# Kernel tuning notes

Measured on AMD Instinct MI355X. Metric: run time of the kernel, lower is better.

## Reference

```python
import jax, jax.numpy as jnp
import numpy as np

N, E = 50000, 800000
F_NODE, F_EDGE, H, LAT, MAXN = 128, 16, 128, 64, 200


def setup_inputs() -> dict:
    key = jax.random.key(0)
    ks = jax.random.split(key, 40)
    s = 0.05
    p = {
        'x': jax.random.normal(ks[0], (N, F_NODE), jnp.float32),
        'edge_index': jax.random.randint(ks[1], (2, E), 0, N, jnp.int64),
        'edge_attr': jax.random.normal(ks[2], (E, F_EDGE), jnp.float32),
        'eps': jax.random.normal(ks[3], (1, LAT), jnp.float32),
        'num_nodes': N,
        # GATConv layer 1 (heads=1)
        'W1': jax.random.normal(ks[4], (F_NODE, H), jnp.float32) * s,
        'att_src1': jax.random.normal(ks[5], (H,), jnp.float32) * s,
        'att_dst1': jax.random.normal(ks[6], (H,), jnp.float32) * s,
        'We1': jax.random.normal(ks[7], (F_EDGE, H), jnp.float32) * s,
        'att_e1': jax.random.normal(ks[8], (H,), jnp.float32) * s,
        'b1': jnp.zeros((H,), jnp.float32),
        # GATConv layer 2
        'W2': jax.random.normal(ks[9], (H, H), jnp.float32) * s,
        'att_src2': jax.random.normal(ks[10], (H,), jnp.float32) * s,
        'att_dst2': jax.random.normal(ks[11], (H,), jnp.float32) * s,
        'We2': jax.random.normal(ks[12], (F_EDGE, H), jnp.float32) * s,
        'att_e2': jax.random.normal(ks[13], (H,), jnp.float32) * s,
        'b2': jnp.zeros((H,), jnp.float32),
        # heads
        'mu_W': jax.random.normal(ks[14], (H, LAT), jnp.float32) * s,
        'mu_b': jnp.zeros((LAT,), jnp.float32),
        'lv_W': jax.random.normal(ks[15], (H, LAT), jnp.float32) * s,
        'lv_b': jnp.zeros((LAT,), jnp.float32),
        'dec_W': jax.random.normal(ks[16], (LAT, H), jnp.float32) * s,
        'dec_b': jnp.zeros((H,), jnp.float32),
        'adj_W1': jax.random.normal(ks[17], (H, H), jnp.float32) * s,
        'adj_b1': jnp.zeros((H,), jnp.float32),
        'adj_W2': jax.random.normal(ks[18], (H, MAXN), jnp.float32) * s,
        'adj_b2': jnp.zeros((MAXN,), jnp.float32),
        'nd_W1': jax.random.normal(ks[19], (H, H), jnp.float32) * s,
        'nd_b1': jnp.zeros((H,), jnp.float32),
        'nd_W2': jax.random.normal(ks[20], (H, F_NODE), jnp.float32) * s,
        'nd_b2': jnp.zeros((F_NODE,), jnp.float32),
    }
    return p


def _gat(h, src, dst, ea, W, a_s, a_d, We, a_e, b, n):
    # PyG GATConv, heads=1: linear transform, per-edge attention, segment softmax over dst
    g = h @ W                                     # [n, H]
    alpha = jax.nn.leaky_relu((g @ a_s)[src] + (g @ a_d)[dst] + (ea @ We) @ a_e,
                              negative_slope=0.2)  # [E']
    m = jax.ops.segment_max(alpha, dst, num_segments=n)
    ex = jnp.exp(alpha - m[dst])
    den = jax.ops.segment_sum(ex, dst, num_segments=n)
    w = ex / den[dst]
    return jax.ops.segment_sum(w[:, None] * g[src], dst, num_segments=n) + b


def _forward(x, edge_index, edge_attr, eps, num_nodes,
             W1, att_src1, att_dst1, We1, att_e1, b1,
             W2, att_src2, att_dst2, We2, att_e2, b2,
             mu_W, mu_b, lv_W, lv_b, dec_W, dec_b,
             adj_W1, adj_b1, adj_W2, adj_b2, nd_W1, nd_b1, nd_W2, nd_b2):
    n = x.shape[0]
    src, dst = edge_index[0], edge_index[1]
    # add self loops; self-loop edge_attr = per-node mean of incoming edge_attr (PyG fill_value='mean')
    deg = jax.ops.segment_sum(jnp.ones((src.shape[0],), x.dtype), dst, num_segments=n)
    mean_ea = jax.ops.segment_sum(edge_attr, dst, num_segments=n) / jnp.maximum(deg, 1.0)[:, None]
    loop = jnp.arange(n)
    src_f = jnp.concatenate([src, loop])
    dst_f = jnp.concatenate([dst, loop])
    ea_f = jnp.concatenate([edge_attr, mean_ea])
    h = jax.nn.relu(_gat(x, src_f, dst_f, ea_f, W1, att_src1, att_dst1, We1, att_e1, b1, n))
    h = jax.nn.relu(_gat(h, src_f, dst_f, ea_f, W2, att_src2, att_dst2, We2, att_e2, b2, n))
    hg = h.mean(axis=0, keepdims=True)            # global_mean_pool, single graph -> [1, H]
    mu = hg @ mu_W + mu_b
    logvar = hg @ lv_W + lv_b
    z = mu + eps * jnp.exp(0.5 * logvar)
    hd = jax.nn.relu(z @ dec_W + dec_b)           # [1, H]
    hn = jnp.broadcast_to(hd[:, None, :], (1, num_nodes, hd.shape[-1]))
    adj = jax.nn.relu(hn @ adj_W1 + adj_b1) @ adj_W2 + adj_b2   # [1, n, MAXN]
    adj = adj[:, :, :num_nodes]
    nodes = jax.nn.relu(hn @ nd_W1 + nd_b1) @ nd_W2 + nd_b2     # [1, n, F_NODE]
    return adj, nodes, mu, logvar


def reference(x, edge_index, edge_attr, eps, num_nodes,
              W1, att_src1, att_dst1, We1, att_e1, b1,
              W2, att_src2, att_dst2, We2, att_e2, b2,
              mu_W, mu_b, lv_W, lv_b, dec_W, dec_b,
              adj_W1, adj_b1, adj_W2, adj_b2, nd_W1, nd_b1, nd_W2, nd_b2):
    return _forward(x, edge_index, edge_attr, eps, num_nodes,
                    W1, att_src1, att_dst1, We1, att_e1, b1,
                    W2, att_src2, att_dst2, We2, att_e2, b2,
                    mu_W, mu_b, lv_W, lv_b, dec_W, dec_b,
                    adj_W1, adj_b1, adj_W2, adj_b2, nd_W1, nd_b1, nd_W2, nd_b2)
```

## Files before the change

kernel.cpp:

```cpp
#include <hip/hip_runtime.h>
#include <math.h>

#define NN   50000
#define EE   800000
#define EF   850000
#define HH   128
#define FE   16
#define LATD 64
#define MAXNN 200

#define ADJ_TOT   10000000
#define NODES_TOT 6400000
#define OUT_TOT   16400000
#define MU_OFF    16400000
#define LV_OFF    16400064

typedef __attribute__((ext_vector_type(8))) short bf16x8;
typedef __attribute__((ext_vector_type(4))) float f32x4;

__device__ __forceinline__ unsigned short f2bf(float f){
  unsigned int u = __float_as_uint(f);
  unsigned int r = (u + 0x7FFFu + ((u>>16)&1u)) >> 16;
  return (unsigned short)r;
}
__device__ __forceinline__ float bf2f(unsigned short h){
  return __uint_as_float(((unsigned int)h)<<16);
}
__device__ __forceinline__ float bflo(unsigned u){ return __uint_as_float(u<<16); }
__device__ __forceinline__ float bfhi(unsigned u){ return __uint_as_float(u & 0xFFFF0000u); }

__global__ void kinit(int* ideg, float* hgsum){
  int i = blockIdx.x*blockDim.x + threadIdx.x;
  if(i < NN) ideg[i]=0;
  if(i < HH) hgsum[i]=0.f;
}

__global__ void kwa(const float* We1, const float* ae1, const float* We2, const float* ae2,
                    float* wa1, float* wa2){
  int t = threadIdx.x;
  if(t < FE){
    float s1=0.f, s2=0.f;
    for(int j=0;j<HH;j++){ s1 += We1[t*HH+j]*ae1[j]; s2 += We2[t*HH+j]*ae2[j]; }
    wa1[t]=s1; wa2[t]=s2;
  }
}

__global__ void kwprep(const float* __restrict__ W1, const float* __restrict__ W2,
                       unsigned short* __restrict__ Wp1, unsigned short* __restrict__ Wp2){
  int t = blockIdx.x*256 + threadIdx.x;
  if(t < HH*HH){
    int n = t >> 7, k = t & 127;
    Wp1[t] = f2bf(W1[k*HH + n]);
    Wp2[t] = f2bf(W2[k*HH + n]);
  }
}

__global__ void kdeg(const int* __restrict__ ei, int* ideg, int* __restrict__ erank){
  int e = blockIdx.x*blockDim.x + threadIdx.x;
  if(e<EE) erank[e] = atomicAdd(&ideg[ei[EE+e]], 1);
}

__global__ void kscan1(const int* __restrict__ ideg, int* rowstart, int* blocksum){
  __shared__ int sd[1024];
  int t=threadIdx.x; int i=blockIdx.x*1024+t;
  int v = (i<NN)? (ideg[i]+1) : 0;
  sd[t]=v; __syncthreads();
  for(int off=1; off<1024; off<<=1){
    int x = (t>=off)? sd[t-off] : 0;
    __syncthreads();
    sd[t] += x;
    __syncthreads();
  }
  if(i<NN) rowstart[i] = sd[t]-v;
  if(t==1023) blocksum[blockIdx.x]=sd[1023];
}
__global__ void kscan2(const int* blocksum, int* blockoff, int nb){
  if(threadIdx.x==0){
    int run=0;
    for(int b=0;b<nb;b++){ blockoff[b]=run; run+=blocksum[b]; }
    blockoff[nb]=run;
  }
}
__global__ void kscan3(int* rowstart, const int* __restrict__ blockoff, int nb){
  int i=blockIdx.x*blockDim.x+threadIdx.x;
  if(i<NN) rowstart[i]+=blockoff[i>>10];
  if(i==0) rowstart[NN]=blockoff[nb];
}

__global__ void kscatter(const int* __restrict__ ei, const float* __restrict__ ea,
                         const float* __restrict__ wa1, const float* __restrict__ wa2,
                         const int* __restrict__ rowstart, const int* __restrict__ erank,
                         float4* __restrict__ csr){
  int e=blockIdx.x*blockDim.x+threadIdx.x;
  if(e>=EE) return;
  int s=ei[e], d=ei[EE+e];
  const float4* ea4 = (const float4*)(ea + (size_t)e*FE);
  float4 v0=ea4[0], v1=ea4[1], v2=ea4[2], v3=ea4[3];
  float va[16]={v0.x,v0.y,v0.z,v0.w, v1.x,v1.y,v1.z,v1.w,
                v2.x,v2.y,v2.z,v2.w, v3.x,v3.y,v3.z,v3.w};
  float d1=0.f,d2=0.f;
  #pragma unroll
  for(int f=0;f<FE;f++){ d1+=va[f]*wa1[f]; d2+=va[f]*wa2[f]; }
  int pos = rowstart[d] + erank[e];
  csr[pos] = make_float4(__int_as_float(s), d1, d2, 0.f);
}

__global__ __launch_bounds__(256) void kself(const int* __restrict__ rowstart,
                      const int* __restrict__ ideg,
                      float4* __restrict__ csr){
  int tid = threadIdx.x;
  int l16 = tid & 15;
  int grp = tid >> 4;
  int i = blockIdx.x*16 + grp;
  if(i>=NN) return;
  int base = rowstart[i]; int deg = ideg[i];
  float s1=0.f, s2=0.f;
  for(int k=l16;k<deg;k+=16){ float4 en=csr[base+k]; s1+=en.y; s2+=en.z; }
  #pragma unroll
  for(int m=8;m>=1;m>>=1){ s1+=__shfl_xor(s1,m,16); s2+=__shfl_xor(s2,m,16); }
  if(l16==0){
    float dg = (float)deg; if(dg<1.f) dg=1.f;
    csr[base+deg] = make_float4(__int_as_float(i), s1/dg, s2/dg, 0.f);
  }
}

__global__ __launch_bounds__(256) void kgemm3(const void* __restrict__ hin, int h_is_fp32,
    const unsigned short* __restrict__ Wp,
    const float* __restrict__ atts, const float* __restrict__ attd,
    unsigned short* __restrict__ Gbf, float* __restrict__ asrc, float* __restrict__ adst){
  int lane = threadIdx.x & 63;
  int wid  = threadIdx.x >> 6;
  int l = lane & 15, q = lane >> 4;
  int r0 = blockIdx.x*64 + wid*16;
  if(r0 >= NN) return;
  const unsigned short* hb = (const unsigned short*)hin;
  const float*          hf = (const float*)hin;
  int row = r0 + l;

  f32x4 acc[8];
  #pragma unroll
  for(int t=0;t<8;t++) acc[t]=(f32x4){0.f,0.f,0.f,0.f};

  #pragma unroll
  for(int kb=0;kb<4;kb++){
    bf16x8 a;
    if(h_is_fp32){
      const float* p = hf + (size_t)row*HH + kb*32 + q*8;
      float4 u0 = *(const float4*)(p);
      float4 u1 = *(const float4*)(p+4);
      a[0]=(short)f2bf(u0.x); a[1]=(short)f2bf(u0.y); a[2]=(short)f2bf(u0.z); a[3]=(short)f2bf(u0.w);
      a[4]=(short)f2bf(u1.x); a[5]=(short)f2bf(u1.y); a[6]=(short)f2bf(u1.z); a[7]=(short)f2bf(u1.w);
    } else {
      a = *(const bf16x8*)(hb + (size_t)row*HH + kb*32 + q*8);
    }
    #pragma unroll
    for(int t=0;t<8;t++){
      bf16x8 b = *(const bf16x8*)(Wp + (size_t)(t*16+l)*HH + kb*32 + q*8);
      acc[t] = __builtin_amdgcn_mfma_f32_16x16x32_bf16(a, b, acc[t], 0,0,0);
    }
  }

  float av[8], dv[8];
  #pragma unroll
  for(int t=0;t<8;t++){ av[t]=atts[t*16+l]; dv[t]=attd[t*16+l]; }
  #pragma unroll
  for(int reg=0;reg<4;reg++){
    float ps=0.f, pd=0.f;
    #pragma unroll
    for(int t=0;t<8;t++){ ps+=acc[t][reg]*av[t]; pd+=acc[t][reg]*dv[t]; }
    #pragma unroll
    for(int m=8;m>=1;m>>=1){ ps+=__shfl_xor(ps,m,16); pd+=__shfl_xor(pd,m,16); }
    if(l==0){ int R=r0+q*4+reg; asrc[R]=ps; adst[R]=pd; }
  }
  #pragma unroll
  for(int t=0;t<8;t++)
    #pragma unroll
    for(int reg=0;reg<4;reg++)
      Gbf[(size_t)(r0+q*4+reg)*HH + t*16 + l] = f2bf(acc[t][reg]);
}

__global__ __launch_bounds__(256) void kgat(const unsigned short* __restrict__ A,
    const float* __restrict__ asrc, const float* __restrict__ adst,
    const int* __restrict__ rowstart, const float4* __restrict__ csr,
    int etsel, const float* __restrict__ bias,
    float* __restrict__ alphabuf, int* __restrict__ srcbuf,
    unsigned short* __restrict__ Bout){
  int lane = threadIdx.x & 63;
  int wid  = threadIdx.x >> 6;
  int i = blockIdx.x*4 + wid;
  if(i >= NN) return;
  int base = rowstart[i]; int len = rowstart[i+1]-base;
  int lq = lane >> 4;
  int lf = lane & 15;
  float adi = adst[i];
  float den;
  float av0=0.f,av1=0.f,av2=0.f,av3=0.f,av4=0.f,av5=0.f,av6=0.f,av7=0.f;

  if(__builtin_expect(len <= 64, 1)){
    float a = -1e30f; int s=0;
    if(lane < len){
      float4 en = csr[base+lane];
      s = __float_as_int(en.x);
      float et = etsel ? en.z : en.y;
      a = asrc[s] + adi + et;
      a = a>0.f ? a : 0.2f*a;
    }
    float m = a;
    #pragma unroll
    for(int mk=32;mk>=1;mk>>=1) m = fmaxf(m, __shfl_xor(m, mk));
    float ex = (lane<len) ? __expf(a-m) : 0.f;
    float sm = ex;
    #pragma unroll
    for(int mk=32;mk>=1;mk>>=1) sm += __shfl_xor(sm, mk);
    den = sm;
    int chunks = (len+3)>>2;
    float wk = __shfl(ex, lq);
    int   sk = __shfl(s, lq);
    uint4 p  = *((const uint4*)(A + (size_t)sk*HH) + lf);
    for(int c=0;c<chunks;c++){
      float wc = wk; uint4 pc = p;
      if(c+1<chunks){
        int idx = (c+1)*4 + lq;
        wk = __shfl(ex, idx);
        sk = __shfl(s, idx);
        p  = *((const uint4*)(A + (size_t)sk*HH) + lf);
      }
      av0 += wc*bflo(pc.x); av1 += wc*bfhi(pc.x);
      av2 += wc*bflo(pc.y); av3 += wc*bfhi(pc.y);
      av4 += wc*bflo(pc.z); av5 += wc*bfhi(pc.z);
      av6 += wc*bflo(pc.w); av7 += wc*bfhi(pc.w);
    }
  } else {
    float lm = -1e30f;
    for(int k=lane;k<len;k+=64){
      float4 en = csr[base+k];
      int s = __float_as_int(en.x);
      float et = etsel ? en.z : en.y;
      float a = asrc[s] + adi + et;
      a = a>0.f ? a : 0.2f*a;
      alphabuf[base+k]=a; srcbuf[base+k]=s;
      lm = fmaxf(lm,a);
    }
    #pragma unroll
    for(int mk=32;mk>=1;mk>>=1) lm = fmaxf(lm, __shfl_xor(lm, mk));
    float ls=0.f;
    for(int k=lane;k<len;k+=64){
      float ex = __expf(alphabuf[base+k]-lm);
      alphabuf[base+k]=ex; ls+=ex;
    }
    #pragma unroll
    for(int mk=32;mk>=1;mk>>=1) ls += __shfl_xor(ls, mk);
    den = ls;
    int chunks = (len+3)>>2;
    for(int c=0;c<chunks;c++){
      int idx = c*4 + lq;
      float wc = (idx<len)? alphabuf[base+idx] : 0.f;
      int   sk = (idx<len)? srcbuf[base+idx] : 0;
      uint4 pc = *((const uint4*)(A + (size_t)sk*HH) + lf);
      av0 += wc*bflo(pc.x); av1 += wc*bfhi(pc.x);
      av2 += wc*bflo(pc.y); av3 += wc*bfhi(pc.y);
      av4 += wc*bflo(pc.z); av5 += wc*bfhi(pc.z);
      av6 += wc*bflo(pc.w); av7 += wc*bfhi(pc.w);
    }
  }
  av0 += __shfl_xor(av0,16); av0 += __shfl_xor(av0,32);
  av1 += __shfl_xor(av1,16); av1 += __shfl_xor(av1,32);
  av2 += __shfl_xor(av2,16); av2 += __shfl_xor(av2,32);
  av3 += __shfl_xor(av3,16); av3 += __shfl_xor(av3,32);
  av4 += __shfl_xor(av4,16); av4 += __shfl_xor(av4,32);
  av5 += __shfl_xor(av5,16); av5 += __shfl_xor(av5,32);
  av6 += __shfl_xor(av6,16); av6 += __shfl_xor(av6,32);
  av7 += __shfl_xor(av7,16); av7 += __shfl_xor(av7,32);
  if(lq==0){
    float inv = 1.f/den;
    float4 b0 = *(const float4*)(bias + lf*8);
    float4 b1 = *(const float4*)(bias + lf*8 + 4);
    float o0 = fmaxf(av0*inv + b0.x, 0.f);
    float o1 = fmaxf(av1*inv + b0.y, 0.f);
    float o2 = fmaxf(av2*inv + b0.z, 0.f);
    float o3 = fmaxf(av3*inv + b0.w, 0.f);
    float o4 = fmaxf(av4*inv + b1.x, 0.f);
    float o5 = fmaxf(av5*inv + b1.y, 0.f);
    float o6 = fmaxf(av6*inv + b1.z, 0.f);
    float o7 = fmaxf(av7*inv + b1.w, 0.f);
    uint4 ov;
    ov.x = (unsigned)f2bf(o0) | ((unsigned)f2bf(o1)<<16);
    ov.y = (unsigned)f2bf(o2) | ((unsigned)f2bf(o3)<<16);
    ov.z = (unsigned)f2bf(o4) | ((unsigned)f2bf(o5)<<16);
    ov.w = (unsigned)f2bf(o6) | ((unsigned)f2bf(o7)<<16);
    *((uint4*)(Bout + (size_t)i*HH) + lf) = ov;
  }
}

__global__ __launch_bounds__(256) void khg(const unsigned short* __restrict__ B, float* hgsum){
  int f = threadIdx.x & 127;
  int half = threadIdx.x >> 7;
  float s=0.f;
  for(int i = blockIdx.x*2+half; i < NN; i += gridDim.x*2)
    s += bf2f(B[(size_t)i*HH + f]);
  __shared__ float sd[256];
  sd[threadIdx.x]=s; __syncthreads();
  if(half==0) atomicAdd(&hgsum[f], sd[threadIdx.x]+sd[threadIdx.x+128]);
}

__global__ __launch_bounds__(256) void kdec(const float* __restrict__ hgsum, const float* __restrict__ eps,
   const float* muW,const float* mub,const float* lvW,const float* lvb,
   const float* decW,const float* decb,
   const float* aW1,const float* ab1,const float* aW2,const float* ab2,
   const float* nW1,const float* nb1,const float* nW2,const float* nb2,
   float* out, float* rowadj, float* rownodes){
  __shared__ float hg[HH], z[LATD], hd[HH], t1[HH], t2[HH];
  int t=threadIdx.x;
  if(t<HH) hg[t]=hgsum[t]*(1.0f/NN);
  __syncthreads();
  if(t<LATD){
    float mu=mub[t], lv=lvb[t];
    for(int k=0;k<HH;k++){ mu += hg[k]*muW[k*LATD+t]; lv += hg[k]*lvW[k*LATD+t]; }
    out[MU_OFF+t]=mu; out[LV_OFF+t]=lv;
    z[t]=mu + eps[t]*expf(0.5f*lv);
  }
  __syncthreads();
  if(t<HH){
    float a=decb[t];
    for(int k=0;k<LATD;k++) a += z[k]*decW[k*HH+t];
    hd[t]=fmaxf(a,0.f);
  }
  __syncthreads();
  if(t<HH){
    float a=ab1[t];
    for(int k=0;k<HH;k++) a += hd[k]*aW1[k*HH+t];
    t1[t]=fmaxf(a,0.f);
  } else {
    int j=t-HH;
    float a=nb1[j];
    for(int k=0;k<HH;k++) a += hd[k]*nW1[k*HH+j];
    t2[j]=fmaxf(a,0.f);
  }
  __syncthreads();
  for(int j=t;j<MAXNN;j+=256){
    float a=ab2[j];
    for(int k=0;k<HH;k++) a += t1[k]*aW2[k*MAXNN+j];
    rowadj[j]=a;
  }
  if(t<HH){
    float a=nb2[t];
    for(int k=0;k<HH;k++) a += t2[k]*nW2[k*HH+t];
    rownodes[t]=a;
  }
}

__global__ __launch_bounds__(256) void kbcast(const float* __restrict__ rowadj,
                                              const float* __restrict__ rownodes,
                                              float* __restrict__ out){
  __shared__ float row[MAXNN+HH];
  int t=threadIdx.x;
  if(t<MAXNN) row[t]=rowadj[t];
  if(t<HH) row[MAXNN+t]=rownodes[t];
  __syncthreads();
  int stride=gridDim.x*blockDim.x;
  for(int idx=blockIdx.x*blockDim.x+t; idx<OUT_TOT; idx+=stride){
    if(idx<ADJ_TOT) out[idx]=row[idx%MAXNN];
    else { int j=(idx-ADJ_TOT)&(HH-1); out[idx]=row[MAXNN+j]; }
  }
}

extern "C" void kernel_launch(void* const* d_in, const int* in_sizes, int n_in,
                              void* d_out, int out_size, void* d_ws, size_t ws_size,
                              hipStream_t stream){
  const float* x   = (const float*)d_in[0];
  const int*   ei  = (const int*)d_in[1];
  const float* ea  = (const float*)d_in[2];
  const float* eps = (const float*)d_in[3];
  const float* W1  =(const float*)d_in[5];
  const float* as1 =(const float*)d_in[6];
  const float* ad1 =(const float*)d_in[7];
  const float* We1 =(const float*)d_in[8];
  const float* ae1 =(const float*)d_in[9];
  const float* b1  =(const float*)d_in[10];
  const float* W2  =(const float*)d_in[11];
  const float* as2 =(const float*)d_in[12];
  const float* ad2 =(const float*)d_in[13];
  const float* We2 =(const float*)d_in[14];
  const float* ae2 =(const float*)d_in[15];
  const float* b2  =(const float*)d_in[16];
  const float* muW =(const float*)d_in[17];
  const float* mub =(const float*)d_in[18];
  const float* lvW =(const float*)d_in[19];
  const float* lvb =(const float*)d_in[20];
  const float* decW=(const float*)d_in[21];
  const float* decb=(const float*)d_in[22];
  const float* aW1 =(const float*)d_in[23];
  const float* ab1 =(const float*)d_in[24];
  const float* aW2 =(const float*)d_in[25];
  const float* ab2 =(const float*)d_in[26];
  const float* nW1 =(const float*)d_in[27];
  const float* nb1 =(const float*)d_in[28];
  const float* nW2 =(const float*)d_in[29];
  const float* nb2 =(const float*)d_in[30];
  float* out=(float*)d_out;

  char* w=(char*)d_ws;
  unsigned short* Abf = (unsigned short*)w; w += (size_t)NN*HH*2;
  unsigned short* Bbf = (unsigned short*)w; w += (size_t)NN*HH*2;
  unsigned short* Wp1 = (unsigned short*)w; w += (size_t)HH*HH*2;
  unsigned short* Wp2 = (unsigned short*)w; w += (size_t)HH*HH*2;
  float4* csr      = (float4*)w; w += (size_t)EF*16;
  float*  alphabuf = (float*)w;  w += (size_t)EF*4;
  int*    srcbuf   = (int*)w;    w += (size_t)EF*4;
  int*    erank    = (int*)w;    w += (size_t)EE*4;
  int*    rowstart = (int*)w;    w += (size_t)(NN+1)*4;
  int*    ideg     = (int*)w;    w += (size_t)NN*4;
  float*  asrc     = (float*)w;  w += (size_t)NN*4;
  float*  adst     = (float*)w;  w += (size_t)NN*4;
  float*  hgsum    = (float*)w;  w += 128*4;
  float*  wa1      = (float*)w;  w += 16*4;
  float*  wa2      = (float*)w;  w += 16*4;
  float*  rowadj   = (float*)w;  w += 256*4;
  float*  rownodes = (float*)w;  w += 128*4;
  int*    blocksum = (int*)w;    w += 64*4;
  int*    blockoff = (int*)w;    w += 64*4;

  int nb = (NN+1023)/1024;
  int gemmblocks = (NN+63)/64;
  int gatblocks  = (NN+3)/4;

  hipLaunchKernelGGL(kinit, dim3((NN+255)/256), dim3(256), 0, stream, ideg, hgsum);
  hipLaunchKernelGGL(kwa, dim3(1), dim3(64), 0, stream, We1, ae1, We2, ae2, wa1, wa2);
  hipLaunchKernelGGL(kwprep, dim3((HH*HH+255)/256), dim3(256), 0, stream, W1, W2, Wp1, Wp2);
  hipLaunchKernelGGL(kdeg, dim3((EE+255)/256), dim3(256), 0, stream, ei, ideg, erank);
  hipLaunchKernelGGL(kscan1, dim3(nb), dim3(1024), 0, stream, ideg, rowstart, blocksum);
  hipLaunchKernelGGL(kscan2, dim3(1), dim3(64), 0, stream, blocksum, blockoff, nb);
  hipLaunchKernelGGL(kscan3, dim3((NN+255)/256), dim3(256), 0, stream, rowstart, blockoff, nb);
  hipLaunchKernelGGL(kscatter, dim3((EE+255)/256), dim3(256), 0, stream,
                     ei, ea, wa1, wa2, rowstart, erank, csr);
  hipLaunchKernelGGL(kself, dim3((NN+15)/16), dim3(256), 0, stream, rowstart, ideg, csr);
  hipLaunchKernelGGL(kgemm3, dim3(gemmblocks), dim3(256), 0, stream,
                     (const void*)x, 1, Wp1, as1, ad1, Abf, asrc, adst);
  hipLaunchKernelGGL(kgat,  dim3(gatblocks), dim3(256), 0, stream, Abf, asrc, adst, rowstart, csr, 0, b1, alphabuf, srcbuf, Bbf);
  hipLaunchKernelGGL(kgemm3, dim3(gemmblocks), dim3(256), 0, stream,
                     (const void*)Bbf, 0, Wp2, as2, ad2, Abf, asrc, adst);
  hipLaunchKernelGGL(kgat,  dim3(gatblocks), dim3(256), 0, stream, Abf, asrc, adst, rowstart, csr, 1, b2, alphabuf, srcbuf, Bbf);
  hipLaunchKernelGGL(khg,   dim3(512), dim3(256), 0, stream, Bbf, hgsum);
  hipLaunchKernelGGL(kdec,  dim3(1), dim3(256), 0, stream, hgsum, eps,
                     muW,mub,lvW,lvb,decW,decb,aW1,ab1,aW2,ab2,nW1,nb1,nW2,nb2,
                     out, rowadj, rownodes);
  hipLaunchKernelGGL(kbcast, dim3(2048), dim3(256), 0, stream, rowadj, rownodes, out);
}
```

Before: 452.8 us.

## Store gathered features in FP8, compact CSR entries, fuse setup kernels

The transformed node features that the GAT aggregation gathers are now stored as FP8 (one byte per element) instead of bf16, which halves the bytes per gathered row. The aggregation lane mapping changes so each lane covers 16 features and eight neighbors are processed per step. CSR entries shrink from 16 to 8 bytes by packing the edge attention terms as bf16, and edge ranks are stored as 16-bit. Three small setup kernels are merged into one launch. FP8 storage lowers the precision of the aggregated features and may hurt accuracy tolerance.

```diff
diff --git a/kernel.cpp b/kernel.cpp
--- a/kernel.cpp
+++ b/kernel.cpp
@@ -17,6 +17,7 @@
 
 typedef __attribute__((ext_vector_type(8))) short bf16x8;
 typedef __attribute__((ext_vector_type(4))) float f32x4;
+typedef __attribute__((ext_vector_type(2))) float f32x2;
 
 __device__ __forceinline__ unsigned short f2bf(float f){
   unsigned int u = __float_as_uint(f);
@@ -26,38 +27,30 @@
 __device__ __forceinline__ float bf2f(unsigned short h){
   return __uint_as_float(((unsigned int)h)<<16);
 }
-__device__ __forceinline__ float bflo(unsigned u){ return __uint_as_float(u<<16); }
-__device__ __forceinline__ float bfhi(unsigned u){ return __uint_as_float(u & 0xFFFF0000u); }
-
-__global__ void kinit(int* ideg, float* hgsum){
+
+__global__ void ksetup(int* ideg, float* hgsum,
+                       const float* We1, const float* ae1, const float* We2, const float* ae2,
+                       float* wa1, float* wa2,
+                       const float* W1, const float* W2,
+                       unsigned short* Wp1, unsigned short* Wp2){
   int i = blockIdx.x*blockDim.x + threadIdx.x;
   if(i < NN) ideg[i]=0;
   if(i < HH) hgsum[i]=0.f;
-}
-
-__global__ void kwa(const float* We1, const float* ae1, const float* We2, const float* ae2,
-                    float* wa1, float* wa2){
-  int t = threadIdx.x;
-  if(t < FE){
+  if(i < FE){
     float s1=0.f, s2=0.f;
-    for(int j=0;j<HH;j++){ s1 += We1[t*HH+j]*ae1[j]; s2 += We2[t*HH+j]*ae2[j]; }
-    wa1[t]=s1; wa2[t]=s2;
-  }
-}
-
-__global__ void kwprep(const float* __restrict__ W1, const float* __restrict__ W2,
-                       unsigned short* __restrict__ Wp1, unsigned short* __restrict__ Wp2){
-  int t = blockIdx.x*256 + threadIdx.x;
-  if(t < HH*HH){
-    int n = t >> 7, k = t & 127;
-    Wp1[t] = f2bf(W1[k*HH + n]);
-    Wp2[t] = f2bf(W2[k*HH + n]);
-  }
-}
-
-__global__ void kdeg(const int* __restrict__ ei, int* ideg, int* __restrict__ erank){
+    for(int j=0;j<HH;j++){ s1 += We1[i*HH+j]*ae1[j]; s2 += We2[i*HH+j]*ae2[j]; }
+    wa1[i]=s1; wa2[i]=s2;
+  }
+  if(i < HH*HH){
+    int n = i >> 7, k = i & 127;
+    Wp1[i] = f2bf(W1[k*HH + n]);
+    Wp2[i] = f2bf(W2[k*HH + n]);
+  }
+}
+
+__global__ void kdeg(const int* __restrict__ ei, int* ideg, unsigned short* __restrict__ erank){
   int e = blockIdx.x*blockDim.x + threadIdx.x;
-  if(e<EE) erank[e] = atomicAdd(&ideg[ei[EE+e]], 1);
+  if(e<EE) erank[e] = (unsigned short)atomicAdd(&ideg[ei[EE+e]], 1);
 }
 
 __global__ void kscan1(const int* __restrict__ ideg, int* rowstart, int* blocksum){
@@ -89,8 +82,8 @@
 
 __global__ void kscatter(const int* __restrict__ ei, const float* __restrict__ ea,
                          const float* __restrict__ wa1, const float* __restrict__ wa2,
-                         const int* __restrict__ rowstart, const int* __restrict__ erank,
-                         float4* __restrict__ csr){
+                         const int* __restrict__ rowstart, const unsigned short* __restrict__ erank,
+                         uint2* __restrict__ csr){
   int e=blockIdx.x*blockDim.x+threadIdx.x;
   if(e>=EE) return;
   int s=ei[e], d=ei[EE+e];
@@ -101,13 +94,15 @@
   float d1=0.f,d2=0.f;
   #pragma unroll
   for(int f=0;f<FE;f++){ d1+=va[f]*wa1[f]; d2+=va[f]*wa2[f]; }
-  int pos = rowstart[d] + erank[e];
-  csr[pos] = make_float4(__int_as_float(s), d1, d2, 0.f);
+  int pos = rowstart[d] + (int)erank[e];
+  uint2 en; en.x = (unsigned)s;
+  en.y = (unsigned)f2bf(d1) | ((unsigned)f2bf(d2)<<16);
+  csr[pos] = en;
 }
 
 __global__ __launch_bounds__(256) void kself(const int* __restrict__ rowstart,
                       const int* __restrict__ ideg,
-                      float4* __restrict__ csr){
+                      uint2* __restrict__ csr){
   int tid = threadIdx.x;
   int l16 = tid & 15;
   int grp = tid >> 4;
@@ -115,19 +110,25 @@
   if(i>=NN) return;
   int base = rowstart[i]; int deg = ideg[i];
   float s1=0.f, s2=0.f;
-  for(int k=l16;k<deg;k+=16){ float4 en=csr[base+k]; s1+=en.y; s2+=en.z; }
+  for(int k=l16;k<deg;k+=16){
+    uint2 en=csr[base+k];
+    s1 += bf2f((unsigned short)(en.y & 0xFFFFu));
+    s2 += bf2f((unsigned short)(en.y >> 16));
+  }
   #pragma unroll
   for(int m=8;m>=1;m>>=1){ s1+=__shfl_xor(s1,m,16); s2+=__shfl_xor(s2,m,16); }
   if(l16==0){
     float dg = (float)deg; if(dg<1.f) dg=1.f;
-    csr[base+deg] = make_float4(__int_as_float(i), s1/dg, s2/dg, 0.f);
+    uint2 en; en.x=(unsigned)i;
+    en.y = (unsigned)f2bf(s1/dg) | ((unsigned)f2bf(s2/dg)<<16);
+    csr[base+deg] = en;
   }
 }
 
 __global__ __launch_bounds__(256) void kgemm3(const void* __restrict__ hin, int h_is_fp32,
     const unsigned short* __restrict__ Wp,
     const float* __restrict__ atts, const float* __restrict__ attd,
-    unsigned short* __restrict__ Gbf, float* __restrict__ asrc, float* __restrict__ adst){
+    unsigned char* __restrict__ A8, float* __restrict__ asrc, float* __restrict__ adst){
   int lane = threadIdx.x & 63;
   int wid  = threadIdx.x >> 6;
   int l = lane & 15, q = lane >> 4;
@@ -175,13 +176,15 @@
   #pragma unroll
   for(int t=0;t<8;t++)
     #pragma unroll
-    for(int reg=0;reg<4;reg++)
-      Gbf[(size_t)(r0+q*4+reg)*HH + t*16 + l] = f2bf(acc[t][reg]);
-}
-
-__global__ __launch_bounds__(256) void kgat(const unsigned short* __restrict__ A,
+    for(int reg=0;reg<4;reg++){
+      int pk = __builtin_amdgcn_cvt_pk_fp8_f32(acc[t][reg], 0.f, 0, false);
+      A8[(size_t)(r0+q*4+reg)*HH + t*16 + l] = (unsigned char)(pk & 0xFF);
+    }
+}
+
+__global__ __launch_bounds__(256) void kgat(const unsigned char* __restrict__ A8,
     const float* __restrict__ asrc, const float* __restrict__ adst,
-    const int* __restrict__ rowstart, const float4* __restrict__ csr,
+    const int* __restrict__ rowstart, const uint2* __restrict__ csr,
     int etsel, const float* __restrict__ bias,
     float* __restrict__ alphabuf, int* __restrict__ srcbuf,
     unsigned short* __restrict__ Bout){
@@ -190,18 +193,20 @@
   int i = blockIdx.x*4 + wid;
   if(i >= NN) return;
   int base = rowstart[i]; int len = rowstart[i+1]-base;
-  int lq = lane >> 4;
-  int lf = lane & 15;
+  int lq = lane >> 3;
+  int lf = lane & 7;
   float adi = adst[i];
   float den;
-  float av0=0.f,av1=0.f,av2=0.f,av3=0.f,av4=0.f,av5=0.f,av6=0.f,av7=0.f;
+  float av[16];
+  #pragma unroll
+  for(int j=0;j<16;j++) av[j]=0.f;
 
   if(__builtin_expect(len <= 64, 1)){
     float a = -1e30f; int s=0;
     if(lane < len){
-      float4 en = csr[base+lane];
-      s = __float_as_int(en.x);
-      float et = etsel ? en.z : en.y;
+      uint2 en = csr[base+lane];
+      s = (int)en.x;
+      float et = etsel ? bf2f((unsigned short)(en.y>>16)) : bf2f((unsigned short)(en.y&0xFFFFu));
       a = asrc[s] + adi + et;
       a = a>0.f ? a : 0.2f*a;
     }
@@ -213,29 +218,34 @@
     #pragma unroll
     for(int mk=32;mk>=1;mk>>=1) sm += __shfl_xor(sm, mk);
     den = sm;
-    int chunks = (len+3)>>2;
+    int chunks = (len+7)>>3;
     float wk = __shfl(ex, lq);
     int   sk = __shfl(s, lq);
-    uint4 p  = *((const uint4*)(A + (size_t)sk*HH) + lf);
+    uint4 p  = *((const uint4*)(A8 + (size_t)sk*HH) + lf);
     for(int c=0;c<chunks;c++){
       float wc = wk; uint4 pc = p;
       if(c+1<chunks){
-        int idx = (c+1)*4 + lq;
+        int idx = (c+1)*8 + lq;
         wk = __shfl(ex, idx);
         sk = __shfl(s, idx);
-        p  = *((const uint4*)(A + (size_t)sk*HH) + lf);
+        p  = *((const uint4*)(A8 + (size_t)sk*HH) + lf);
       }
-      av0 += wc*bflo(pc.x); av1 += wc*bfhi(pc.x);
-      av2 += wc*bflo(pc.y); av3 += wc*bfhi(pc.y);
-      av4 += wc*bflo(pc.z); av5 += wc*bfhi(pc.z);
-      av6 += wc*bflo(pc.w); av7 += wc*bfhi(pc.w);
+      f32x2 v;
+      v=__builtin_amdgcn_cvt_pk_f32_fp8(pc.x,false); av[0]+=wc*v[0];  av[1]+=wc*v[1];
+      v=__builtin_amdgcn_cvt_pk_f32_fp8(pc.x,true ); av[2]+=wc*v[0];  av[3]+=wc*v[1];
+      v=__builtin_amdgcn_cvt_pk_f32_fp8(pc.y,false); av[4]+=wc*v[0];  av[5]+=wc*v[1];
+      v=__builtin_amdgcn_cvt_pk_f32_fp8(pc.y,true ); av[6]+=wc*v[0];  av[7]+=wc*v[1];
+      v=__builtin_amdgcn_cvt_pk_f32_fp8(pc.z,false); av[8]+=wc*v[0];  av[9]+=wc*v[1];
+      v=__builtin_amdgcn_cvt_pk_f32_fp8(pc.z,true ); av[10]+=wc*v[0]; av[11]+=wc*v[1];
+      v=__builtin_amdgcn_cvt_pk_f32_fp8(pc.w,false); av[12]+=wc*v[0]; av[13]+=wc*v[1];
+      v=__builtin_amdgcn_cvt_pk_f32_fp8(pc.w,true ); av[14]+=wc*v[0]; av[15]+=wc*v[1];
     }
   } else {
     float lm = -1e30f;
     for(int k=lane;k<len;k+=64){
-      float4 en = csr[base+k];
-      int s = __float_as_int(en.x);
-      float et = etsel ? en.z : en.y;
+      uint2 en = csr[base+k];
+      int s = (int)en.x;
+      float et = etsel ? bf2f((unsigned short)(en.y>>16)) : bf2f((unsigned short)(en.y&0xFFFFu));
       float a = asrc[s] + adi + et;
       a = a>0.f ? a : 0.2f*a;
       alphabuf[base+k]=a; srcbuf[base+k]=s;
@@ -251,44 +261,53 @@
     #pragma unroll
     for(int mk=32;mk>=1;mk>>=1) ls += __shfl_xor(ls, mk);
     den = ls;
-    int chunks = (len+3)>>2;
+    int chunks = (len+7)>>3;
     for(int c=0;c<chunks;c++){
-      int idx = c*4 + lq;
+      int idx = c*8 + lq;
       float wc = (idx<len)? alphabuf[base+idx] : 0.f;
       int   sk = (idx<len)? srcbuf[base+idx] : 0;
-      uint4 pc = *((const uint4*)(A + (size_t)sk*HH) + lf);
-      av0 += wc*bflo(pc.x); av1 += wc*bfhi(pc.x);
-      av2 += wc*bflo(pc.y); av3 += wc*bfhi(pc.y);
-      av4 += wc*bflo(pc.z); av5 += wc*bfhi(pc.z);
-      av6 += wc*bflo(pc.w); av7 += wc*bfhi(pc.w);
-    }
-  }
-  av0 += __shfl_xor(av0,16); av0 += __shfl_xor(av0,32);
-  av1 += __shfl_xor(av1,16); av1 += __shfl_xor(av1,32);
-  av2 += __shfl_xor(av2,16); av2 += __shfl_xor(av2,32);
-  av3 += __shfl_xor(av3,16); av3 += __shfl_xor(av3,32);
-  av4 += __shfl_xor(av4,16); av4 += __shfl_xor(av4,32);
-  av5 += __shfl_xor(av5,16); av5 += __shfl_xor(av5,32);
-  av6 += __shfl_xor(av6,16); av6 += __shfl_xor(av6,32);
-  av7 += __shfl_xor(av7,16); av7 += __shfl_xor(av7,32);
+      uint4 pc = *((const uint4*)(A8 + (size_t)sk*HH) + lf);
+      f32x2 v;
+      v=__builtin_amdgcn_cvt_pk_f32_fp8(pc.x,false); av[0]+=wc*v[0];  av[1]+=wc*v[1];
+      v=__builtin_amdgcn_cvt_pk_f32_fp8(pc.x,true ); av[2]+=wc*v[0];  av[3]+=wc*v[1];
+      v=__builtin_amdgcn_cvt_pk_f32_fp8(pc.y,false); av[4]+=wc*v[0];  av[5]+=wc*v[1];
+      v=__builtin_amdgcn_cvt_pk_f32_fp8(pc.y,true ); av[6]+=wc*v[0];  av[7]+=wc*v[1];
+      v=__builtin_amdgcn_cvt_pk_f32_fp8(pc.z,false); av[8]+=wc*v[0];  av[9]+=wc*v[1];
+      v=__builtin_amdgcn_cvt_pk_f32_fp8(pc.z,true ); av[10]+=wc*v[0]; av[11]+=wc*v[1];
+      v=__builtin_amdgcn_cvt_pk_f32_fp8(pc.w,false); av[12]+=wc*v[0]; av[13]+=wc*v[1];
+      v=__builtin_amdgcn_cvt_pk_f32_fp8(pc.w,true ); av[14]+=wc*v[0]; av[15]+=wc*v[1];
+    }
+  }
+  #pragma unroll
+  for(int j=0;j<16;j++){
+    av[j] += __shfl_xor(av[j],8);
+    av[j] += __shfl_xor(av[j],16);
+    av[j] += __shfl_xor(av[j],32);
+  }
   if(lq==0){
     float inv = 1.f/den;
-    float4 b0 = *(const float4*)(bias + lf*8);
-    float4 b1 = *(const float4*)(bias + lf*8 + 4);
-    float o0 = fmaxf(av0*inv + b0.x, 0.f);
-    float o1 = fmaxf(av1*inv + b0.y, 0.f);
-    float o2 = fmaxf(av2*inv + b0.z, 0.f);
-    float o3 = fmaxf(av3*inv + b0.w, 0.f);
-    float o4 = fmaxf(av4*inv + b1.x, 0.f);
-    float o5 = fmaxf(av5*inv + b1.y, 0.f);
-    float o6 = fmaxf(av6*inv + b1.z, 0.f);
-    float o7 = fmaxf(av7*inv + b1.w, 0.f);
-    uint4 ov;
-    ov.x = (unsigned)f2bf(o0) | ((unsigned)f2bf(o1)<<16);
-    ov.y = (unsigned)f2bf(o2) | ((unsigned)f2bf(o3)<<16);
-    ov.z = (unsigned)f2bf(o4) | ((unsigned)f2bf(o5)<<16);
-    ov.w = (unsigned)f2bf(o6) | ((unsigned)f2bf(o7)<<16);
-    *((uint4*)(Bout + (size_t)i*HH) + lf) = ov;
+    const float4* bp = (const float4*)(bias + lf*16);
+    float4 b0=bp[0], b1=bp[1], b2=bp[2], b3=bp[3];
+    float o[16];
+    o[0] =fmaxf(av[0] *inv+b0.x,0.f); o[1] =fmaxf(av[1] *inv+b0.y,0.f);
+    o[2] =fmaxf(av[2] *inv+b0.z,0.f); o[3] =fmaxf(av[3] *inv+b0.w,0.f);
+    o[4] =fmaxf(av[4] *inv+b1.x,0.f); o[5] =fmaxf(av[5] *inv+b1.y,0.f);
+    o[6] =fmaxf(av[6] *inv+b1.z,0.f); o[7] =fmaxf(av[7] *inv+b1.w,0.f);
+    o[8] =fmaxf(av[8] *inv+b2.x,0.f); o[9] =fmaxf(av[9] *inv+b2.y,0.f);
+    o[10]=fmaxf(av[10]*inv+b2.z,0.f); o[11]=fmaxf(av[11]*inv+b2.w,0.f);
+    o[12]=fmaxf(av[12]*inv+b3.x,0.f); o[13]=fmaxf(av[13]*inv+b3.y,0.f);
+    o[14]=fmaxf(av[14]*inv+b3.z,0.f); o[15]=fmaxf(av[15]*inv+b3.w,0.f);
+    uint4 ov1, ov2;
+    ov1.x=(unsigned)f2bf(o[0]) |((unsigned)f2bf(o[1]) <<16);
+    ov1.y=(unsigned)f2bf(o[2]) |((unsigned)f2bf(o[3]) <<16);
+    ov1.z=(unsigned)f2bf(o[4]) |((unsigned)f2bf(o[5]) <<16);
+    ov1.w=(unsigned)f2bf(o[6]) |((unsigned)f2bf(o[7]) <<16);
+    ov2.x=(unsigned)f2bf(o[8]) |((unsigned)f2bf(o[9]) <<16);
+    ov2.y=(unsigned)f2bf(o[10])|((unsigned)f2bf(o[11])<<16);
+    ov2.z=(unsigned)f2bf(o[12])|((unsigned)f2bf(o[13])<<16);
+    ov2.w=(unsigned)f2bf(o[14])|((unsigned)f2bf(o[15])<<16);
+    uint4* outp = (uint4*)(Bout + (size_t)i*HH + lf*16);
+    outp[0]=ov1; outp[1]=ov2;
   }
 }
 
@@ -400,14 +419,14 @@
   float* out=(float*)d_out;
 
   char* w=(char*)d_ws;
-  unsigned short* Abf = (unsigned short*)w; w += (size_t)NN*HH*2;
+  unsigned char*  A8  = (unsigned char*)w;  w += (size_t)NN*HH;
   unsigned short* Bbf = (unsigned short*)w; w += (size_t)NN*HH*2;
   unsigned short* Wp1 = (unsigned short*)w; w += (size_t)HH*HH*2;
   unsigned short* Wp2 = (unsigned short*)w; w += (size_t)HH*HH*2;
-  float4* csr      = (float4*)w; w += (size_t)EF*16;
+  uint2*  csr      = (uint2*)w;  w += (size_t)EF*8;
   float*  alphabuf = (float*)w;  w += (size_t)EF*4;
   int*    srcbuf   = (int*)w;    w += (size_t)EF*4;
-  int*    erank    = (int*)w;    w += (size_t)EE*4;
+  unsigned short* erank = (unsigned short*)w; w += (size_t)EE*2;
   int*    rowstart = (int*)w;    w += (size_t)(NN+1)*4;
   int*    ideg     = (int*)w;    w += (size_t)NN*4;
   float*  asrc     = (float*)w;  w += (size_t)NN*4;
@@ -424,9 +443,8 @@
   int gemmblocks = (NN+63)/64;
   int gatblocks  = (NN+3)/4;
 
-  hipLaunchKernelGGL(kinit, dim3((NN+255)/256), dim3(256), 0, stream, ideg, hgsum);
-  hipLaunchKernelGGL(kwa, dim3(1), dim3(64), 0, stream, We1, ae1, We2, ae2, wa1, wa2);
-  hipLaunchKernelGGL(kwprep, dim3((HH*HH+255)/256), dim3(256), 0, stream, W1, W2, Wp1, Wp2);
+  hipLaunchKernelGGL(ksetup, dim3((NN+255)/256), dim3(256), 0, stream,
+                     ideg, hgsum, We1, ae1, We2, ae2, wa1, wa2, W1, W2, Wp1, Wp2);
   hipLaunchKernelGGL(kdeg, dim3((EE+255)/256), dim3(256), 0, stream, ei, ideg, erank);
   hipLaunchKernelGGL(kscan1, dim3(nb), dim3(1024), 0, stream, ideg, rowstart, blocksum);
   hipLaunchKernelGGL(kscan2, dim3(1), dim3(64), 0, stream, blocksum, blockoff, nb);
@@ -435,11 +453,11 @@
                      ei, ea, wa1, wa2, rowstart, erank, csr);
   hipLaunchKernelGGL(kself, dim3((NN+15)/16), dim3(256), 0, stream, rowstart, ideg, csr);
   hipLaunchKernelGGL(kgemm3, dim3(gemmblocks), dim3(256), 0, stream,
-                     (const void*)x, 1, Wp1, as1, ad1, Abf, asrc, adst);
-  hipLaunchKernelGGL(kgat,  dim3(gatblocks), dim3(256), 0, stream, Abf, asrc, adst, rowstart, csr, 0, b1, alphabuf, srcbuf, Bbf);
+                     (const void*)x, 1, Wp1, as1, ad1, A8, asrc, adst);
+  hipLaunchKernelGGL(kgat,  dim3(gatblocks), dim3(256), 0, stream, A8, asrc, adst, rowstart, csr, 0, b1, alphabuf, srcbuf, Bbf);
   hipLaunchKernelGGL(kgemm3, dim3(gemmblocks), dim3(256), 0, stream,
-                     (const void*)Bbf, 0, Wp2, as2, ad2, Abf, asrc, adst);
-  hipLaunchKernelGGL(kgat,  dim3(gatblocks), dim3(256), 0, stream, Abf, asrc, adst, rowstart, csr, 1, b2, alphabuf, srcbuf, Bbf);
+                     (const void*)Bbf, 0, Wp2, as2, ad2, A8, asrc, adst);
+  hipLaunchKernelGGL(kgat,  dim3(gatblocks), dim3(256), 0, stream, A8, asrc, adst, rowstart, csr, 1, b2, alphabuf, srcbuf, Bbf);
   hipLaunchKernelGGL(khg,   dim3(512), dim3(256), 0, stream, Bbf, hgsum);
   hipLaunchKernelGGL(kdec,  dim3(1), dim3(256), 0, stream, hgsum, eps,
                      muW,mub,lvW,lvb,decW,decb,aW1,ab1,aW2,ab2,nW1,nb1,nW2,nb2,
```

Result: no change. 445.5 us (-1.6%).
